# Kernel optimization log

Measured on AMD Instinct MI355X. Metric: run time of the kernel, lower is better.

## Reference

```python
import jax, jax.numpy as jnp
import numpy as np

B, C, D, H, W = 2, 64, 3, 96, 96
CD = C * D  # conv1x1 channel count = in_dim * 3


def setup_inputs() -> dict:
    key = jax.random.key(0)
    ks = jax.random.split(key, 7)
    s = 1.0 / np.sqrt(CD)
    x = jax.random.normal(ks[0], (B, C, D, H, W), dtype=jnp.float32)
    Wq = jax.random.uniform(ks[1], (CD, CD), jnp.float32, -s, s)
    bq = jax.random.uniform(ks[2], (CD,), jnp.float32, -s, s)
    Wk = jax.random.uniform(ks[3], (CD, CD), jnp.float32, -s, s)
    bk = jax.random.uniform(ks[4], (CD,), jnp.float32, -s, s)
    Wv = jax.random.uniform(ks[5], (CD, CD), jnp.float32, -s, s)
    bv = jax.random.uniform(ks[6], (CD,), jnp.float32, -s, s)
    return {"x": x, "Wq": Wq, "bq": bq, "Wk": Wk, "bk": bk, "Wv": Wv, "bv": bv}


def reference(x, Wq, bq, Wk, bk, Wv, bv):
    b, c, d, h, w = x.shape
    n = h * w
    xr = x.reshape(b, c * d, n)  # [B, CD, N]; conv1x1 == channel matmul
    q = jnp.einsum('oc,bcn->bon', Wq, xr) + bq[:, None]  # [B, CD, N]
    k = jnp.einsum('oc,bcn->bon', Wk, xr) + bk[:, None]
    v = jnp.einsum('oc,bcn->bon', Wv, xr) + bv[:, None]
    energy = jnp.einsum('bcn,bcm->bnm', q, k)            # [B, N, N]
    attention = jax.nn.softmax(energy, axis=-1)
    # out = bmm(value, attention^T): out[b,c,m] = sum_n v[b,c,n] * attn[b,m,n]
    out = jnp.einsum('bcn,bmn->bcm', v, attention)       # [B, CD, N]
    return out.reshape(b, c, d, h, w)
```

## Files before the change

kernel.cpp:

```cpp
#include <hip/hip_runtime.h>

#define NSEQ  9216
#define CDIM  192
#define LOG2E 1.44269504088896f

typedef _Float16 h8_t  __attribute__((ext_vector_type(8)));
typedef _Float16 h4_t  __attribute__((ext_vector_type(4)));
typedef _Float16 h2_t  __attribute__((ext_vector_type(2)));
typedef __fp16   fp16x2 __attribute__((ext_vector_type(2)));
typedef float    f4_t  __attribute__((ext_vector_type(4)));
typedef float    f16v  __attribute__((ext_vector_type(16)));
typedef unsigned u32x2 __attribute__((ext_vector_type(2)));

static __device__ inline unsigned f2u(float f) { union { float f; unsigned u; } x; x.f = f; return x.u; }
static __device__ inline float u2f(unsigned u) { union { unsigned u; float f; } x; x.u = u; return x.f; }

static __device__ inline unsigned cvt_pk(float a, float b) {
    union { fp16x2 h; unsigned u; } x;
    x.h = __builtin_amdgcn_cvt_pkrtz(a, b);
    return x.u;
}

static __device__ inline u32x2 plswap(unsigned a, unsigned b) {
    return __builtin_amdgcn_permlane32_swap(a, b, false, false);
}

static __device__ inline void gl_lds16(const _Float16* g, _Float16* l) {
    __builtin_amdgcn_global_load_lds(
        (const __attribute__((address_space(1))) void*)g,
        (__attribute__((address_space(3))) void*)l,
        16, 0, 0);
}

__global__ __launch_bounds__(256) void wconv_kernel(
    const float* __restrict__ Wq, const float* __restrict__ Wk,
    const float* __restrict__ Wv, _Float16* __restrict__ Wh)
{
    int i = blockIdx.x * 256 + threadIdx.x;
    if (i >= 3 * 9216) return;
    const float* src = (i < 9216) ? Wq : (i < 18432 ? Wk : Wv);
    float s = (i < 9216) ? LOG2E : 1.f;
    int r = i % 9216;
    f4_t w = ((const f4_t*)src)[r];
    h4_t h = {(_Float16)(w[0]*s), (_Float16)(w[1]*s),
              (_Float16)(w[2]*s), (_Float16)(w[3]*s)};
    ((h4_t*)Wh)[i] = h;
}

__global__ __launch_bounds__(384) void proj_kernel(
    const float* __restrict__ x, const _Float16* __restrict__ Wh,
    const float* __restrict__ bq, const float* __restrict__ bk,
    const float* __restrict__ bv,
    _Float16* __restrict__ QT, _Float16* __restrict__ KT, _Float16* __restrict__ Vg)
{
    __shared__ __align__(16) _Float16 Xs[32 * 200];

    const int tid  = threadIdx.x;
    const int lane = tid & 63, wave = tid >> 6;
    const int L31  = lane & 31, hi = lane >> 5;
    const int b    = blockIdx.x / 288;
    const int n0   = (blockIdx.x % 288) * 32;

    {
        const int nn = tid & 31;
        const int c0 = (tid >> 5) * 16;
        const float* xp = x + (size_t)(b * CDIM + c0) * NSEQ + n0 + nn;
        _Float16 tmp[16];
        #pragma unroll
        for (int j = 0; j < 16; j++)
            tmp[j] = (_Float16)xp[(size_t)j * NSEQ];
        #pragma unroll
        for (int g = 0; g < 4; g++) {
            h4_t h = {tmp[4*g], tmp[4*g+1], tmp[4*g+2], tmp[4*g+3]};
            *(h4_t*)(Xs + nn * 200 + c0 + 4 * g) = h;
        }
    }
    __syncthreads();

    const int mat = wave >> 1;
    const int sh  = (wave & 1) * 3;
    const int n   = n0 + L31;

    h8_t bf[12];
    #pragma unroll
    for (int t = 0; t < 12; t++)
        bf[t] = *(const h8_t*)(Xs + L31 * 200 + t * 16 + hi * 8);

    const _Float16* W = Wh + mat * CDIM * CDIM;
    const float* bias = (mat == 0) ? bq : (mat == 1 ? bk : bv);
    const float bscale = (mat == 0) ? LOG2E : 1.f;

    f16v acc[3];
    #pragma unroll
    for (int s = 0; s < 3; s++)
        #pragma unroll
        for (int r = 0; r < 16; r++) acc[s][r] = 0.f;

    #pragma unroll
    for (int t = 0; t < 12; t++) {
        #pragma unroll
        for (int s = 0; s < 3; s++) {
            h8_t a = *(const h8_t*)(W + ((sh + s) * 32 + L31) * CDIM + t * 16 + hi * 8);
            acc[s] = __builtin_amdgcn_mfma_f32_32x32x16_f16(a, bf[t], acc[s], 0, 0, 0);
        }
    }

    if (mat < 2) {
        _Float16* dst = ((mat == 0) ? QT : KT) + ((size_t)b * NSEQ + n) * CDIM;
        #pragma unroll
        for (int s = 0; s < 3; s++) {
            #pragma unroll
            for (int g = 0; g < 4; g++) {
                f4_t bb = *(const f4_t*)&bias[(sh + s) * 32 + 8 * g + 4 * hi];
                h4_t h = {(_Float16)(acc[s][4*g+0] + bb[0] * bscale),
                          (_Float16)(acc[s][4*g+1] + bb[1] * bscale),
                          (_Float16)(acc[s][4*g+2] + bb[2] * bscale),
                          (_Float16)(acc[s][4*g+3] + bb[3] * bscale)};
                *(h4_t*)(dst + (sh + s) * 32 + 8 * g + 4 * hi) = h;
            }
        }
    } else {
        #pragma unroll
        for (int s = 0; s < 3; s++) {
            #pragma unroll
            for (int g = 0; g < 4; g++) {
                f4_t bb = *(const f4_t*)&bias[(sh + s) * 32 + 8 * g + 4 * hi];
                #pragma unroll
                for (int r = 0; r < 4; r++) {
                    int o = (sh + s) * 32 + 8 * g + 4 * hi + r;
                    Vg[((size_t)b * CDIM + o) * NSEQ + n] =
                        (_Float16)(acc[s][4*g+r] + bb[r]);
                }
            }
        }
    }
}

template<int NSPLIT>
__global__ __launch_bounds__(256, 2) void flash_kernel(
    const _Float16* __restrict__ QT, const _Float16* __restrict__ KTg,
    const _Float16* __restrict__ Vg,
    _Float16* __restrict__ O_part, float* __restrict__ m_part, float* __restrict__ l_part)
{
    constexpr int TKI  = NSEQ / 32;
    constexpr int base = TKI / NSPLIT, rem = TKI % NSPLIT;
    __shared__ __align__(16) _Float16 Sh[25600];

    const int tid  = threadIdx.x;
    const int lane = tid & 63, wave = tid >> 6;
    const int L31  = lane & 31, hi = lane >> 5;
    const int qtile = blockIdx.x, split = blockIdx.y, b = blockIdx.z;
    const int q0 = qtile * 128 + wave * 32;

    const int nk     = base + (split < rem ? 1 : 0);
    const int kstart = split * base + (split < rem ? split : rem);

    h8_t qf[12];
    const _Float16* qbase = QT + ((size_t)b * NSEQ + q0 + L31) * CDIM + hi * 8;
    #pragma unroll
    for (int t = 0; t < 12; t++) qf[t] = *(const h8_t*)(qbase + t * 16);

    f16v acc[6];
    #pragma unroll
    for (int s = 0; s < 6; s++)
        #pragma unroll
        for (int r = 0; r < 16; r++) acc[s][r] = 0.f;
    float m_run = -__builtin_inff();
    float l_run = 0.f;

    const _Float16* ksrc = KTg + ((size_t)b * NSEQ + kstart * 32) * CDIM;
    const _Float16* vsrc = Vg + (size_t)b * CDIM * NSEQ + kstart * 32;

    const int k7 = L31 & 7;
    int ka[12];
    #pragma unroll
    for (int t = 0; t < 12; t++) {
        int p = 2 * t + hi + k7; if (p >= 24) p -= 24;
        ka[t] = L31 * 384 + p * 16;
    }
    const int r2 = L31 >> 1;
    const int va0 = L31 * 64 + (((hi + r2) & 3) * 16);
    const int va1 = L31 * 64 + (((2 + hi + r2) & 3) * 16);

    const _Float16 *kp[3], *vp[3];
    #pragma unroll
    for (int r = 0; r < 3; r++) {
        int i = r * 256 + tid;
        int row = i / 24, pp = i % 24;
        int c = pp - (row & 7); if (c < 0) c += 24;
        kp[r] = ksrc + row * CDIM + c * 8;
        int cv = i >> 2, s = i & 3;
        int g = (s - (cv >> 1)) & 3;
        vp[r] = vsrc + (size_t)cv * NSEQ + g * 8;
    }

    auto stage = [&](int kbB, int vbB) {
        #pragma unroll
        for (int r = 0; r < 3; r++) {
            int off = (r * 256 + wave * 64) * 16;
            gl_lds16(kp[r], (_Float16*)((char*)Sh + kbB + off));
            gl_lds16(vp[r], (_Float16*)((char*)Sh + vbB + off));
        }
        #pragma unroll
        for (int r = 0; r < 3; r++) { kp[r] += 32 * CDIM; vp[r] += 32; }
    };

    stage(0, 24576);
    __syncthreads();

    auto body = [&](int kt, int KB, int VB, int KW, int VW) {
        if (kt + 1 < nk) stage(KW, VW);

        f16v st;
        #pragma unroll
        for (int r = 0; r < 16; r++) st[r] = 0.f;
        #pragma unroll
        for (int t = 0; t < 12; t++) {
            h8_t a = *(const h8_t*)((char*)Sh + KB + ka[t]);
            st = __builtin_amdgcn_mfma_f32_32x32x16_f16(a, qf[t], st, 0, 0, 0);
        }

        float a0 = fmaxf(fmaxf(st[0], st[1]),  st[2]);
        float a1 = fmaxf(fmaxf(st[3], st[4]),  st[5]);
        float a2 = fmaxf(fmaxf(st[6], st[7]),  st[8]);
        float a3 = fmaxf(fmaxf(st[9], st[10]), st[11]);
        float a4 = fmaxf(fmaxf(st[12], st[13]), st[14]);
        float mx = fmaxf(fmaxf(fmaxf(a0, a1), fmaxf(a2, a3)), fmaxf(a4, st[15]));
        u32x2 mxw = plswap(f2u(mx), f2u(mx));
        mx = fmaxf(u2f(mxw[0]), u2f(mxw[1]));

        if (__builtin_expect(__any(mx > m_run + 9.f), 0)) {
            float m_new = fmaxf(m_run, mx);
            float alpha = __builtin_exp2f(m_run - m_new);
            l_run *= alpha;
            #pragma unroll
            for (int cs = 0; cs < 6; cs++)
                #pragma unroll
                for (int r = 0; r < 16; r++) acc[cs][r] *= alpha;
            m_run = m_new;
        }

        unsigned pu[8];
        float ps0 = 0.f, ps1 = 0.f;
        #pragma unroll
        for (int t2 = 0; t2 < 8; t2++) {
            float e0 = __builtin_exp2f(st[2*t2]   - m_run);
            float e1 = __builtin_exp2f(st[2*t2+1] - m_run);
            ps0 += e0; ps1 += e1;
            pu[t2] = cvt_pk(e0, e1);
        }
        l_run += ps0 + ps1;

        union { h8_t h; unsigned u[4]; } pb0, pb1;
        u32x2 x0 = plswap(pu[0], pu[2]);
        u32x2 x1 = plswap(pu[1], pu[3]);
        u32x2 x2 = plswap(pu[4], pu[6]);
        u32x2 x3 = plswap(pu[5], pu[7]);
        pb0.u[0] = x0[0]; pb0.u[1] = x1[0]; pb0.u[2] = x0[1]; pb0.u[3] = x1[1];
        pb1.u[0] = x2[0]; pb1.u[1] = x3[0]; pb1.u[2] = x2[1]; pb1.u[3] = x3[1];

        #pragma unroll
        for (int ks = 0; ks < 2; ks++) {
            h8_t pb = ks ? pb1.h : pb0.h;
            int vaof = ks ? va1 : va0;
            #pragma unroll
            for (int cs = 0; cs < 6; cs++) {
                h8_t va = *(const h8_t*)((char*)Sh + VB + cs * 2048 + vaof);
                acc[cs] = __builtin_amdgcn_mfma_f32_32x32x16_f16(va, pb, acc[cs], 0, 0, 0);
            }
        }

        __syncthreads();
    };

    int kt = 0;
    for (; kt + 1 < nk; kt += 2) {
        body(kt,     0,     24576, 12288, 36864);
        body(kt + 1, 12288, 36864, 0,     24576);
    }
    if (kt < nk)
        body(kt, 0, 24576, 12288, 36864);

    u32x2 lw = plswap(f2u(l_run), f2u(l_run));
    float l_tot = u2f(lw[0]) + u2f(lw[1]);
    const size_t pw = (size_t)(b * NSPLIT + split) * NSEQ + q0;
    if (lane < 32) {
        m_part[pw + lane] = m_run;
        l_part[pw + lane] = l_tot;
    }
    _Float16* T = Sh + wave * 6400;
    #pragma unroll
    for (int cs = 0; cs < 6; cs++)
        #pragma unroll
        for (int g = 0; g < 4; g++) {
            h4_t hh = {(_Float16)acc[cs][4*g+0], (_Float16)acc[cs][4*g+1],
                       (_Float16)acc[cs][4*g+2], (_Float16)acc[cs][4*g+3]};
            *(h4_t*)(T + L31 * 200 + cs * 32 + 8 * g + 4 * hi) = hh;
        }
    _Float16* ob = O_part + pw * CDIM;
    #pragma unroll
    for (int it = 0; it < 12; it++) {
        int i = it * 64 + lane;
        int qq = i / 24, col = i % 24;
        h8_t h = *(const h8_t*)(T + qq * 200 + col * 8);
        *(h8_t*)(ob + (size_t)qq * CDIM + col * 8) = h;
    }
}

template<int NS>
__global__ __launch_bounds__(256) void combine_kernel(
    const _Float16* __restrict__ O_part, const float* __restrict__ m_part,
    const float* __restrict__ l_part, float* __restrict__ out)
{
    __shared__ float Cs[CDIM][33];
    __shared__ float winv[NS][32];
    const int tid = threadIdx.x;
    const int b  = blockIdx.y;
    const int n0 = blockIdx.x * 32;

    if (tid < 32) {
        int n = n0 + tid;
        float mm[NS], ll[NS], ms = -__builtin_inff();
        #pragma unroll
        for (int s = 0; s < NS; s++) {
            mm[s] = m_part[(b * NS + s) * NSEQ + n];
            ll[s] = l_part[(b * NS + s) * NSEQ + n];
            ms = fmaxf(ms, mm[s]);
        }
        float denom = 0.f;
        #pragma unroll
        for (int s = 0; s < NS; s++) {
            float w = __builtin_exp2f(mm[s] - ms);
            mm[s] = w;
            denom += w * ll[s];
        }
        #pragma unroll
        for (int s = 0; s < NS; s++) winv[s][tid] = mm[s] / denom;
    }
    __syncthreads();

    for (int i = tid; i < 32 * 24; i += 256) {
        int nl = i / 24, cp = i % 24;
        float v[8];
        #pragma unroll
        for (int j = 0; j < 8; j++) v[j] = 0.f;
        #pragma unroll
        for (int s = 0; s < NS; s++) {
            h8_t op = *(const h8_t*)(O_part +
                ((size_t)(b * NS + s) * NSEQ + n0 + nl) * CDIM + cp * 8);
            float w = winv[s][nl];
            #pragma unroll
            for (int j = 0; j < 8; j++) v[j] += w * (float)op[j];
        }
        #pragma unroll
        for (int j = 0; j < 8; j++) Cs[cp * 8 + j][nl] = v[j];
    }
    __syncthreads();
    for (int i = tid; i < CDIM * 32; i += 256) {
        int nl = i & 31, c = i >> 5;
        out[((size_t)b * CDIM + c) * NSEQ + n0 + nl] = Cs[c][nl];
    }
}

extern "C" void kernel_launch(void* const* d_in, const int* in_sizes, int n_in,
                              void* d_out, int out_size, void* d_ws, size_t ws_size,
                              hipStream_t stream)
{
    const float* x  = (const float*)d_in[0];
    const float* Wq = (const float*)d_in[1];
    const float* bq = (const float*)d_in[2];
    const float* Wk = (const float*)d_in[3];
    const float* bk = (const float*)d_in[4];
    const float* Wv = (const float*)d_in[5];
    const float* bv = (const float*)d_in[6];
    float* out = (float*)d_out;

    char* ws = (char*)d_ws;
    _Float16* QT = (_Float16*)(ws);
    _Float16* KT = (_Float16*)(ws + 7077888);
    _Float16* Vg = (_Float16*)(ws + 14155776);
    char* tail = ws + 21233664;
    _Float16* Wh = (_Float16*)tail;
    _Float16* O_part = (_Float16*)tail;

    wconv_kernel<<<108, 256, 0, stream>>>(Wq, Wk, Wv, Wh);
    proj_kernel<<<576, 384, 0, stream>>>(x, Wh, bq, bk, bv, QT, KT, Vg);

    const size_t need7 = 21233664ull + 7 * 7077888ull + 2 * 516096ull;
    const size_t need4 = 21233664ull + 4 * 7077888ull + 2 * 294912ull;
    if (ws_size >= need7) {
        float* m_part = (float*)(tail + 7 * 7077888ull);
        float* l_part = (float*)(tail + 7 * 7077888ull + 516096ull);
        flash_kernel<7><<<dim3(72, 7, 2), 256, 0, stream>>>(QT, KT, Vg, O_part, m_part, l_part);
        combine_kernel<7><<<dim3(288, 2), 256, 0, stream>>>(O_part, m_part, l_part, out);
    } else if (ws_size >= need4) {
        float* m_part = (float*)(tail + 4 * 7077888ull);
        float* l_part = (float*)(tail + 4 * 7077888ull + 294912ull);
        flash_kernel<4><<<dim3(72, 4, 2), 256, 0, stream>>>(QT, KT, Vg, O_part, m_part, l_part);
        combine_kernel<4><<<dim3(288, 2), 256, 0, stream>>>(O_part, m_part, l_part, out);
    } else {
        float* m_part = (float*)(tail + 2 * 7077888ull);
        float* l_part = (float*)(tail + 2 * 7077888ull + 147456ull);
        flash_kernel<2><<<dim3(72, 2, 2), 256, 0, stream>>>(QT, KT, Vg, O_part, m_part, l_part);
        combine_kernel<2><<<dim3(288, 2), 256, 0, stream>>>(O_part, m_part, l_part, out);
    }
}
```

Before: 269.4 us.

## Stage V tiles through registers into padded LDS layout instead of direct global-to-LDS

V tiles are no longer copied with direct global-to-LDS loads using a swizzled layout. They are now prefetched one tile ahead into registers and written to LDS with a padded row stride of 40 halves, which avoids bank conflicts without the swizzle. The V read address simplifies and LDS use grows slightly. This adds register pressure and explicit LDS store instructions inside the loop, which can hurt occupancy or issue throughput.

```diff
diff --git a/kernel.cpp b/kernel.cpp
--- a/kernel.cpp
+++ b/kernel.cpp
@@ -144,7 +144,8 @@
 {
     constexpr int TKI  = NSEQ / 32;
     constexpr int base = TKI / NSPLIT, rem = TKI % NSPLIT;
-    __shared__ __align__(16) _Float16 Sh[25600];
+    constexpr int VB0  = 12288, VB1 = 19968;
+    __shared__ __align__(16) _Float16 Sh[27648];
 
     const int tid  = threadIdx.x;
     const int lane = tid & 63, wave = tid >> 6;
@@ -178,38 +179,57 @@
         int p = 2 * t + hi + k7; if (p >= 24) p -= 24;
         ka[t] = L31 * 384 + p * 16;
     }
-    const int r2 = L31 >> 1;
-    const int va0 = L31 * 64 + (((hi + r2) & 3) * 16);
-    const int va1 = L31 * 64 + (((2 + hi + r2) & 3) * 16);
-
-    const _Float16 *kp[3], *vp[3];
+    const int va0 = L31 * 40 + hi * 8;
+
+    const _Float16* kp[3];
     #pragma unroll
     for (int r = 0; r < 3; r++) {
         int i = r * 256 + tid;
         int row = i / 24, pp = i % 24;
         int c = pp - (row & 7); if (c < 0) c += 24;
         kp[r] = ksrc + row * CDIM + c * 8;
-        int cv = i >> 2, s = i & 3;
-        int g = (s - (cv >> 1)) & 3;
-        vp[r] = vsrc + (size_t)cv * NSEQ + g * 8;
-    }
-
-    auto stage = [&](int kbB, int vbB) {
+    }
+    int vds[3];
+    const _Float16* vgl[3];
+    #pragma unroll
+    for (int r = 0; r < 3; r++) {
+        int i = r * 256 + tid;
+        int c = i >> 2, seg = i & 3;
+        vds[r] = c * 40 + seg * 8;
+        vgl[r] = vsrc + (size_t)c * NSEQ + seg * 8;
+    }
+
+    auto stageK = [&](int kbB) {
         #pragma unroll
         for (int r = 0; r < 3; r++) {
             int off = (r * 256 + wave * 64) * 16;
             gl_lds16(kp[r], (_Float16*)((char*)Sh + kbB + off));
-            gl_lds16(vp[r], (_Float16*)((char*)Sh + vbB + off));
-        }
-        #pragma unroll
-        for (int r = 0; r < 3; r++) { kp[r] += 32 * CDIM; vp[r] += 32; }
+            kp[r] += 32 * CDIM;
+        }
     };
 
-    stage(0, 24576);
+    h8_t vreg[3];
+    #pragma unroll
+    for (int r = 0; r < 3; r++) { vreg[r] = *(const h8_t*)(vgl[r]); vgl[r] += 32; }
+    stageK(0);
+    #pragma unroll
+    for (int r = 0; r < 3; r++) *(h8_t*)(Sh + VB0 + vds[r]) = vreg[r];
+    if (nk > 1) {
+        #pragma unroll
+        for (int r = 0; r < 3; r++) { vreg[r] = *(const h8_t*)(vgl[r]); vgl[r] += 32; }
+    }
     __syncthreads();
 
-    auto body = [&](int kt, int KB, int VB, int KW, int VW) {
-        if (kt + 1 < nk) stage(KW, VW);
+    auto body = [&](int kt, int KB, int VBc, int KW, int VWc) {
+        if (kt + 1 < nk) {
+            #pragma unroll
+            for (int r = 0; r < 3; r++) *(h8_t*)(Sh + VWc + vds[r]) = vreg[r];
+            stageK(KW);
+        }
+        if (kt + 2 < nk) {
+            #pragma unroll
+            for (int r = 0; r < 3; r++) { vreg[r] = *(const h8_t*)(vgl[r]); vgl[r] += 32; }
+        }
 
         f16v st;
         #pragma unroll
@@ -262,10 +282,9 @@
         #pragma unroll
         for (int ks = 0; ks < 2; ks++) {
             h8_t pb = ks ? pb1.h : pb0.h;
-            int vaof = ks ? va1 : va0;
             #pragma unroll
             for (int cs = 0; cs < 6; cs++) {
-                h8_t va = *(const h8_t*)((char*)Sh + VB + cs * 2048 + vaof);
+                h8_t va = *(const h8_t*)(Sh + VBc + cs * 1280 + va0 + ks * 16);
                 acc[cs] = __builtin_amdgcn_mfma_f32_32x32x16_f16(va, pb, acc[cs], 0, 0, 0);
             }
         }
@@ -275,11 +294,11 @@
 
     int kt = 0;
     for (; kt + 1 < nk; kt += 2) {
-        body(kt,     0,     24576, 12288, 36864);
-        body(kt + 1, 12288, 36864, 0,     24576);
+        body(kt,     0,     VB0, 12288, VB1);
+        body(kt + 1, 12288, VB1, 0,     VB0);
     }
     if (kt < nk)
-        body(kt, 0, 24576, 12288, 36864);
+        body(kt, 0, VB0, 12288, VB1);
 
     u32x2 lw = plswap(f2u(l_run), f2u(l_run));
     float l_tot = u2f(lw[0]) + u2f(lw[1]);
```

Measured after the change: 277.1 us. 2.9% more time.

## Triple-buffer K/V tiles in LDS with vmcnt-based waits instead of full syncs

Applied to the files above, without the earlier changes.

Replaces the double-buffered K/V staging with a three-slot ring buffer, prefetching two tiles ahead and rotating buffer offsets each iteration. It swaps __syncthreads for explicit s_waitcnt vmcnt plus s_barrier, so loads for the tile after next stay in flight while the current tile is computed. The aim is to hide more global-to-LDS latency. LDS per block grows from 50 KB to 72 KB, which may reduce occupancy at two blocks per CU. The hand-counted vmcnt values depend on the compiler emitting no other outstanding vector memory operations.

```diff
diff --git a/kernel.cpp b/kernel.cpp
--- a/kernel.cpp
+++ b/kernel.cpp
@@ -144,7 +144,9 @@
 {
     constexpr int TKI  = NSEQ / 32;
     constexpr int base = TKI / NSPLIT, rem = TKI % NSPLIT;
-    __shared__ __align__(16) _Float16 Sh[25600];
+    constexpr int BUF  = 24576;
+    static_assert(base >= 2, "prologue assumes >=2 tiles");
+    __shared__ __align__(16) _Float16 Sh[3 * 12288];
 
     const int tid  = threadIdx.x;
     const int lane = tid & 63, wave = tid >> 6;
@@ -178,9 +180,9 @@
         int p = 2 * t + hi + k7; if (p >= 24) p -= 24;
         ka[t] = L31 * 384 + p * 16;
     }
-    const int r2 = L31 >> 1;
-    const int va0 = L31 * 64 + (((hi + r2) & 3) * 16);
-    const int va1 = L31 * 64 + (((2 + hi + r2) & 3) * 16);
+    const int q2 = L31 >> 1;
+    const int va0 = 12288 + L31 * 64 + (((hi + q2) & 3) * 16);
+    const int va1 = 12288 + L31 * 64 + (((2 + hi + q2) & 3) * 16);
 
     const _Float16 *kp[3], *vp[3];
     #pragma unroll
@@ -194,29 +196,32 @@
         vp[r] = vsrc + (size_t)cv * NSEQ + g * 8;
     }
 
-    auto stage = [&](int kbB, int vbB) {
+    auto stage = [&](int bb) {
         #pragma unroll
         for (int r = 0; r < 3; r++) {
             int off = (r * 256 + wave * 64) * 16;
-            gl_lds16(kp[r], (_Float16*)((char*)Sh + kbB + off));
-            gl_lds16(vp[r], (_Float16*)((char*)Sh + vbB + off));
+            gl_lds16(kp[r], (_Float16*)((char*)Sh + bb + off));
+            gl_lds16(vp[r], (_Float16*)((char*)Sh + bb + 12288 + off));
         }
         #pragma unroll
         for (int r = 0; r < 3; r++) { kp[r] += 32 * CDIM; vp[r] += 32; }
     };
 
-    stage(0, 24576);
-    __syncthreads();
-
-    auto body = [&](int kt, int KB, int VB, int KW, int VW) {
-        if (kt + 1 < nk) stage(KW, VW);
+    int b0 = 0, b1 = BUF, b2 = 2 * BUF;
+    stage(b0);
+    stage(b1);
+    asm volatile("s_waitcnt vmcnt(6)" ::: "memory");
+    __builtin_amdgcn_s_barrier();
+
+    for (int kt = 0; kt < nk; ++kt) {
+        if (kt + 2 < nk) stage(b2);
 
         f16v st;
         #pragma unroll
         for (int r = 0; r < 16; r++) st[r] = 0.f;
         #pragma unroll
         for (int t = 0; t < 12; t++) {
-            h8_t a = *(const h8_t*)((char*)Sh + KB + ka[t]);
+            h8_t a = *(const h8_t*)((char*)Sh + b0 + ka[t]);
             st = __builtin_amdgcn_mfma_f32_32x32x16_f16(a, qf[t], st, 0, 0, 0);
         }
 
@@ -265,21 +270,18 @@
             int vaof = ks ? va1 : va0;
             #pragma unroll
             for (int cs = 0; cs < 6; cs++) {
-                h8_t va = *(const h8_t*)((char*)Sh + VB + cs * 2048 + vaof);
+                h8_t va = *(const h8_t*)((char*)Sh + b0 + cs * 2048 + vaof);
                 acc[cs] = __builtin_amdgcn_mfma_f32_32x32x16_f16(va, pb, acc[cs], 0, 0, 0);
             }
         }
 
-        __syncthreads();
-    };
-
-    int kt = 0;
-    for (; kt + 1 < nk; kt += 2) {
-        body(kt,     0,     24576, 12288, 36864);
-        body(kt + 1, 12288, 36864, 0,     24576);
-    }
-    if (kt < nk)
-        body(kt, 0, 24576, 12288, 36864);
+        if (kt + 1 < nk) {
+            if (kt + 2 < nk) asm volatile("s_waitcnt vmcnt(6)" ::: "memory");
+            else             asm volatile("s_waitcnt vmcnt(0)" ::: "memory");
+            __builtin_amdgcn_s_barrier();
+        }
+        int tmp = b0; b0 = b1; b1 = b2; b2 = tmp;
+    }
 
     u32x2 lw = plswap(f2u(l_run), f2u(l_run));
     float l_tot = u2f(lw[0]) + u2f(lw[1]);
@@ -288,6 +290,7 @@
         m_part[pw + lane] = m_run;
         l_part[pw + lane] = l_tot;
     }
+    __syncthreads();
     _Float16* T = Sh + wave * 6400;
     #pragma unroll
     for (int cs = 0; cs < 6; cs++)
```

Measured after the change: 269.0 us. Within noise of the previous version (-0.1%).
